# Optimization experiments

Measured on AMD Instinct MI355X. Metric: run time of the kernel, lower is better.

## Reference

```python
import jax, jax.numpy as jnp
import numpy as np

C = 64          # num_channels
NB = 8          # num_bessel
NE = 10         # num_elements
N_NODES = 20000
N_EDGES = 320000

def _silu_norm():
    # e3nn normalize2mom constant for silu: 1/sqrt(E[silu(Z)^2]), Z~N(0,1)
    x, w = np.polynomial.hermite.hermgauss(100)
    z = np.sqrt(2.0) * x
    f = z / (1.0 + np.exp(-z))
    m2 = float(np.sum(w * f * f) / np.sqrt(np.pi))
    return np.float32(1.0 / np.sqrt(m2))

C_SILU = _silu_norm()
SQRT3 = np.float32(np.sqrt(3.0))
SQRT2 = np.float32(np.sqrt(2.0))
INV_SQRT_C = np.float32(1.0 / np.sqrt(C))
INV_SQRT_2C = np.float32(1.0 / np.sqrt(2 * C))
INV_SQRT_3C = np.float32(1.0 / np.sqrt(3 * C))
INV_SQRT_NB = np.float32(1.0 / np.sqrt(NB))
INV_SQRT_64 = np.float32(1.0 / np.sqrt(64.0))


def setup_inputs() -> dict:
    key = jax.random.key(0)
    ks = jax.random.split(key, 22)
    n = lambda k, s: jax.random.normal(k, s, dtype=jnp.float32)
    return {
        "node_feats": n(ks[0], (N_NODES, 4 * C)),
        "edge_feats": jax.random.uniform(ks[1], (N_EDGES, NB), dtype=jnp.float32),
        "edge_attrs": n(ks[2], (N_EDGES, 4)),
        "iedges": jax.random.randint(ks[3], (N_EDGES,), 0, N_NODES),
        "jedges": jax.random.randint(ks[4], (N_EDGES,), 0, N_NODES),
        "atomic_numbers": jax.random.randint(ks[5], (N_NODES,), 0, NE),
        "Wup0": n(ks[6], (C, C)), "Wup1": n(ks[7], (C, C)),
        "Wm1": n(ks[8], (NB, 64)), "Wm2": n(ks[9], (64, 64)),
        "Wm3": n(ks[10], (64, 64)), "Wm4": n(ks[11], (64, 5 * C)),
        "Wl0": n(ks[12], (2 * C, C)), "Wl1": n(ks[13], (3 * C, C)),
        "Ws0c1": n(ks[14], (NE, 1, C)), "Ws0c2": n(ks[15], (NE, 2, C)),
        "Ws0c3": n(ks[16], (NE, 2, C)),
        "Ws1c1": n(ks[17], (NE, 1, C)), "Ws1c2": n(ks[18], (NE, 1, C)),
        "Ws1c3": n(ks[19], (NE, 2, C)),
        "Wp0": n(ks[20], (C, C)), "Wp1": n(ks[21], (C, C)),
    }


def reference(node_feats, edge_feats, edge_attrs, iedges, jedges, atomic_numbers,
              Wup0, Wup1, Wm1, Wm2, Wm3, Wm4, Wl0, Wl1,
              Ws0c1, Ws0c2, Ws0c3, Ws1c1, Ws1c2, Ws1c3, Wp0, Wp1):
    Nn = node_feats.shape[0]
    # split irreps: C scalars (0e) then C vectors (1e), channel-major layout
    s = node_feats[:, :C]                       # (N, C)
    v = node_feats[:, C:].reshape(Nn, C, 3)     # (N, C, 3)

    # linear_up: per-l channel mixing, fan-in normalized (e3nn o3.Linear)
    s = (s @ Wup0) * INV_SQRT_C
    v = jnp.einsum('ncm,ck->nkm', v, Wup1) * INV_SQRT_C

    # conv_tp_weights: e3nn FullyConnectedNet [8,64,64,64,5C] with silu
    h = jax.nn.silu(edge_feats @ (Wm1 * INV_SQRT_NB)) * C_SILU
    h = jax.nn.silu(h @ (Wm2 * INV_SQRT_64)) * C_SILU
    h = jax.nn.silu(h @ (Wm3 * INV_SQRT_64)) * C_SILU
    tpw = h @ (Wm4 * INV_SQRT_64)               # (E, 5C)

    # gather sender node features per edge
    xs = s[iedges]                              # (E, C)
    xv = v[iedges]                              # (E, C, 3)
    eas = edge_attrs[:, 0:1]                    # (E, 1) scalar edge attr
    eav = edge_attrs[:, 1:4]                    # (E, 3) vector edge attr

    # 5 uvu CG paths (component-normalized e3nn TensorProduct):
    wa, wb = tpw[:, 0:C], tpw[:, C:2 * C]
    wc, wd, we = tpw[:, 2 * C:3 * C], tpw[:, 3 * C:4 * C], tpw[:, 4 * C:5 * C]
    m0 = wa * xs * eas                                              # 0e x 0e -> 0e
    m1 = wb * jnp.einsum('ecm,em->ec', xv, eav) / SQRT3             # 1e x 1e -> 0e
    m2 = (wc * xs)[:, :, None] * eav[:, None, :]                    # 0e x 1e -> 1e
    m3 = (wd * eas)[:, :, None] * xv                                # 1e x 0e -> 1e
    m4 = we[:, :, None] * jnp.cross(xv, eav[:, None, :]) / SQRT2    # 1e x 1e -> 1e

    # scatter-sum messages to receiver nodes
    msg_s = jax.ops.segment_sum(jnp.concatenate([m0, m1], axis=1), jedges, num_segments=Nn)        # (N, 2C)
    msg_v = jax.ops.segment_sum(jnp.concatenate([m2, m3, m4], axis=1), jedges, num_segments=Nn)    # (N, 3C, 3)

    # linear: middle irreps (2C x 0e + 3C x 1e) -> C x (0e + 1e)
    s2 = (msg_s @ Wl0) * INV_SQRT_2C            # (N, C)
    v2 = jnp.einsum('ncm,ck->nkm', msg_v, Wl1) * INV_SQRT_3C  # (N, C, 3)

    # symmetric (ACE/MACE) contraction, correlation=3, element-dependent weights
    w01 = Ws0c1[atomic_numbers, 0]              # (N, C)
    w02 = Ws0c2[atomic_numbers]                 # (N, 2, C)
    w03 = Ws0c3[atomic_numbers]                 # (N, 2, C)
    w11 = Ws1c1[atomic_numbers, 0]
    w12 = Ws1c2[atomic_numbers, 0]
    w13 = Ws1c3[atomic_numbers]
    vv = jnp.sum(v2 * v2, axis=-1)              # (N, C) = |v|^2 per channel
    out_s = (w01 * s2 + w02[:, 0] * s2 * s2 + w02[:, 1] * vv / SQRT3
             + w03[:, 0] * s2 * s2 * s2 + w03[:, 1] * s2 * vv / SQRT3)
    coef_v = w11 + w12 * s2 + w13[:, 0] * s2 * s2 + w13[:, 1] * vv / SQRT3
    out_v = coef_v[:, :, None] * v2             # (N, C, 3)

    # linearproduct
    so = (out_s @ Wp0) * INV_SQRT_C
    vo = jnp.einsum('ncm,ck->nkm', out_v, Wp1) * INV_SQRT_C
    return jnp.concatenate([so, vo.reshape(Nn, 3 * C)], axis=1)   # (N, 4C)
```

## Files before the change

kernel.cpp:

```cpp
#include <hip/hip_runtime.h>


typedef unsigned short u16;
typedef unsigned int u32;
typedef __attribute__((ext_vector_type(8))) short bf16x8;
typedef __attribute__((ext_vector_type(4))) float f32x4;

#define CW_UP0 0
#define CW_UP1 4096
#define CW_M1  8192
#define CW_M2  8704
#define CW_M3  12800
#define CW_M4  16896
#define CW_L0  37376
#define CW_L1  45568
#define CW_P0  57856
#define CW_P1  61952
#define CW_S01 66048
#define CW_S02 66688
#define CW_S03 67968
#define CW_S11 69248
#define CW_S12 69888
#define CW_S13 70528
#define CW_TOTAL 71808

#define C_SILU     1.6765224f
#define INV_SQRT3  0.57735027f
#define INV_SQRT2  0.70710678f
#define SC_L1      0.35355339f
#define SC_L234    0.125f

#define HS16 72
#define NFRAG 116
#define FW0 60
#define FW1 76
#define FP0 100
#define FP1 108
#define TP 88

__device__ __forceinline__ float b2f(u16 u) {
  union { u32 i; float f; } x; x.i = ((u32)u) << 16; return x.f;
}
__device__ __forceinline__ u16 f2b(float f) {
  union { float f; u32 i; } x; x.f = f;
  u32 i = x.i;
  u32 r = (i + 0x7fffu + ((i >> 16) & 1u)) >> 16;
  return (u16)r;
}
__device__ __forceinline__ float ldf(const void* p, size_t i, int f32) {
  return f32 ? ((const float*)p)[i] : b2f(((const u16*)p)[i]);
}
__device__ __forceinline__ float silu_n(float x) {
  return C_SILU * x / (1.0f + __expf(-x));
}

__global__ void k_detect(const void* nf, int* flag, int* deg, int nN) {
  __shared__ int cnt;
  if (threadIdx.x == 0) cnt = 0;
  __syncthreads();
  const u16* p = (const u16*)nf;
  int wild = 0;
  for (int i = threadIdx.x; i < 4096; i += 256) {
    float ax = fabsf(b2f(p[i]));
    if (!(ax <= 1e10f) || (ax != 0.f && ax < 1e-10f)) wild++;
  }
  atomicAdd(&cnt, wild);
  for (int i = threadIdx.x; i < nN; i += 256) deg[i] = 0;
  __syncthreads();
  if (threadIdx.x == 0) *flag = (cnt > 100) ? 1 : 0;
}

struct WPtrs { const void* p[16]; };

__global__ __launch_bounds__(256) void k_front(
    WPtrs wp, float* __restrict__ cw, u16* __restrict__ bwH,
    u16* __restrict__ bwL, const int* __restrict__ je, int* __restrict__ deg,
    const void* __restrict__ nf, float* __restrict__ sup,
    float* __restrict__ vup, int nN, int nE, int nb0,
    const int* __restrict__ flagp) {
  __shared__ float row[16][256];
  const int f32 = *flagp;
  int bid = blockIdx.x, tid = threadIdx.x;

  if (bid < 281) {
    const int   sizes[16]  = {4096,4096,512,4096,4096,20480,8192,12288,4096,
                              4096,640,1280,1280,640,640,1280};
    const float scales[16] = {0.125f,0.125f,0.35355339f,0.125f,0.125f,0.125f,
                              0.08838835f,0.07216878f,0.125f,0.125f,
                              1.f,1.f,1.f,1.f,1.f,1.f};
    int gid = bid * 256 + tid;
    if (gid >= CW_TOTAL) return;
    int off = gid, seg = 0;
    while (off >= sizes[seg]) { off -= sizes[seg]; seg++; }
    cw[gid] = ldf(wp.p[seg], off, f32) * scales[seg];
  } else if (bid < 513) {
    int gid = (bid - 281) * 256 + tid;
    int f = gid >> 9, idx = gid & 511;
    int l = idx >> 3, j = idx & 7;
    int q = l >> 4, col16 = l & 15;
    float v = 0.f;
    if (f < 4) {
      int k = q * 8 + j, n = f * 16 + col16;
      if (k < 8) v = ldf(wp.p[2], (size_t)k * 64 + n, f32);
    } else if (f < 20) {
      const void* w = (f < 12) ? wp.p[3] : wp.p[4];
      int t = (f < 12) ? f - 4 : f - 12;
      int n = (t >> 1) * 16 + col16, ks = t & 1;
      int k = ks * 32 + q * 8 + j;
      v = ldf(w, (size_t)k * 64 + n, f32);
    } else if (f < 60) {
      int t = f - 20;
      int n = (t >> 1) * 16 + col16, ks = t & 1;
      int k = ks * 32 + q * 8 + j;
      v = ldf(wp.p[5], (size_t)k * 320 + n, f32);
    } else if (f < 76) {
      int t = f - FW0, ks = t >> 2, n = t & 3;
      int k = ks * 32 + q * 8 + j;
      v = ldf(wp.p[6], (size_t)k * 64 + n * 16 + col16, f32) * 0.08838835f;
    } else if (f < 100) {
      int t = f - FW1, ks = t >> 2, n = t & 3;
      int k = ks * 32 + q * 8 + j;
      v = ldf(wp.p[7], (size_t)k * 64 + n * 16 + col16, f32) * 0.07216878f;
    } else if (f < 108) {
      int t = f - FP0, ks = t >> 2, n = t & 3;
      int k = ks * 32 + q * 8 + j;
      v = ldf(wp.p[8], (size_t)k * 64 + n * 16 + col16, f32) * 0.125f;
    } else {
      int t = f - FP1, ks = t >> 2, n = t & 3;
      int k = ks * 32 + q * 8 + j;
      v = ldf(wp.p[9], (size_t)k * 64 + n * 16 + col16, f32) * 0.125f;
    }
    u16 hi = f2b(v);
    u16 lo = f2b(v - b2f(hi));
    size_t o = (size_t)f * 512 + (size_t)l * 8 + j;
    bwH[o] = hi;
    bwL[o] = lo;
  } else if (bid < nb0) {
    int e = (bid - 513) * 256 + tid;
    if (e < nE) atomicAdd(&deg[je[e]], 1);
  } else {
    int w = tid >> 6, l = tid & 63;
    int nb = (bid - nb0) * 16 + w * 4;
#pragma unroll
    for (int nl = 0; nl < 4; nl++) {
      int n = nb + nl;
      int nn = n < nN ? n : 0;
#pragma unroll
      for (int t = 0; t < 4; t++)
        row[w * 4 + nl][t * 64 + l] = ldf(nf, (size_t)nn * 256 + t * 64 + l, f32);
    }
    float sacc[4] = {0.f, 0.f, 0.f, 0.f};
    float v0[4] = {0.f, 0.f, 0.f, 0.f};
    float v1[4] = {0.f, 0.f, 0.f, 0.f};
    float v2[4] = {0.f, 0.f, 0.f, 0.f};
#pragma unroll 4
    for (int c = 0; c < 64; c++) {
      float w0 = ldf(wp.p[0], (size_t)c * 64 + l, f32);
      float w1 = ldf(wp.p[1], (size_t)c * 64 + l, f32);
#pragma unroll
      for (int nl = 0; nl < 4; nl++) {
        const float* rw = row[w * 4 + nl];
        sacc[nl] += rw[c] * w0;
        v0[nl] += rw[64 + c * 3 + 0] * w1;
        v1[nl] += rw[64 + c * 3 + 1] * w1;
        v2[nl] += rw[64 + c * 3 + 2] * w1;
      }
    }
#pragma unroll
    for (int nl = 0; nl < 4; nl++) {
      int n = nb + nl;
      if (n < nN) {
        sup[(size_t)n * 64 + l] = sacc[nl] * 0.125f;
        vup[((size_t)n * 3 + 0) * 64 + l] = v0[nl] * 0.125f;
        vup[((size_t)n * 3 + 1) * 64 + l] = v1[nl] * 0.125f;
        vup[((size_t)n * 3 + 2) * 64 + l] = v2[nl] * 0.125f;
      }
    }
  }
}

__global__ __launch_bounds__(256) void k_scan(const int* __restrict__ deg,
                                              int* __restrict__ offs,
                                              int* __restrict__ cursor, int nN) {
  __shared__ int wsum[8];
  int t = threadIdx.x;
  int lane = t & 63, wv = t >> 6;
  int base = 0;
  for (int c0 = 0; c0 < nN; c0 += 256) {
    int i = c0 + t;
    int v = (i < nN) ? deg[i] : 0;
    int s = v;
#pragma unroll
    for (int off = 1; off < 64; off <<= 1) {
      int x = __shfl_up(s, off);
      if (lane >= off) s += x;
    }
    if (lane == 63) wsum[wv] = s;
    __syncthreads();
    if (t == 0) {
      int r = 0;
#pragma unroll
      for (int ww = 0; ww < 4; ww++) { int x = wsum[ww]; wsum[ww] = r; r += x; }
      wsum[4] = r;
    }
    __syncthreads();
    int excl = base + wsum[wv] + s - v;
    if (i < nN) { offs[i] = excl; cursor[i] = excl; }
    base += wsum[4];
    __syncthreads();
  }
  if (t == 0) offs[nN] = base;
}

__global__ __launch_bounds__(256) void k_scatter2(
    const int* __restrict__ je, const int* __restrict__ ie,
    const void* __restrict__ ea, const void* __restrict__ ef,
    int* __restrict__ cursor, int* __restrict__ iSlot,
    float4* __restrict__ eaSlot, float4* __restrict__ efSlot, int nE,
    const int* __restrict__ flagp) {
  const int f32 = *flagp;
  int e = blockIdx.x * 256 + threadIdx.x;
  if (e >= nE) return;
  int pos = atomicAdd(&cursor[je[e]], 1);
  iSlot[pos] = ie[e];
  float4 av;
  float4 f0, f1;
  if (f32) {
    av = ((const float4*)ea)[e];
    f0 = ((const float4*)ef)[(size_t)e * 2];
    f1 = ((const float4*)ef)[(size_t)e * 2 + 1];
  } else {
    uint2 r = ((const uint2*)ea)[e];
    av = make_float4(b2f(r.x & 0xffff), b2f(r.x >> 16),
                     b2f(r.y & 0xffff), b2f(r.y >> 16));
    uint4 u = ((const uint4*)ef)[e];
    f0 = make_float4(b2f(u.x & 0xffff), b2f(u.x >> 16),
                     b2f(u.y & 0xffff), b2f(u.y >> 16));
    f1 = make_float4(b2f(u.z & 0xffff), b2f(u.z >> 16),
                     b2f(u.w & 0xffff), b2f(u.w >> 16));
  }
  eaSlot[pos] = av;
  efSlot[(size_t)pos * 2] = f0;
  efSlot[(size_t)pos * 2 + 1] = f1;
}

__global__ __launch_bounds__(192) void k_mlp4(
    const float4* __restrict__ efSlot, const int* __restrict__ offs,
    const u16* __restrict__ bwH, const u16* __restrict__ bwL,
    u16* __restrict__ tpw, int gn0, int gn1, int capEff) {
  __shared__ u16 H[3][64 * HS16];
  int tid = threadIdx.x;
  int w = tid >> 6, l = tid & 63;
  int m = l & 15, q = l >> 4;
  int base = offs[gn0];
  int cnt = offs[gn1] - base;
  int lim = cnt < capEff ? cnt : capEff;
  int tb = (blockIdx.x * 3 + w) * 64;
  if (tb >= lim) return;
  u16* Hw = H[w];

  bf16x8 zero8 = {0,0,0,0,0,0,0,0};
  bf16x8 A1h[4], A1l[4];
#pragma unroll
  for (int t = 0; t < 4; t++) { A1h[t] = zero8; A1l[t] = zero8; }
  if (q == 0) {
#pragma unroll
    for (int t = 0; t < 4; t++) {
      int s = tb + t * 16 + m; if (s > lim - 1) s = lim - 1;
      float4 q0 = efSlot[((size_t)(base + s)) * 2];
      float4 q1 = efSlot[((size_t)(base + s)) * 2 + 1];
      float v[8] = {q0.x, q0.y, q0.z, q0.w, q1.x, q1.y, q1.z, q1.w};
      bf16x8 hi, lo;
#pragma unroll
      for (int j = 0; j < 8; j++) {
        u16 h = f2b(v[j]);
        hi[j] = (short)h;
        lo[j] = (short)f2b(v[j] - b2f(h));
      }
      A1h[t] = hi; A1l[t] = lo;
    }
  }
#pragma unroll
  for (int n = 0; n < 4; n++) {
    bf16x8 Bh = *(const bf16x8*)(bwH + (size_t)n * 512 + (size_t)l * 8);
    bf16x8 Bl = *(const bf16x8*)(bwL + (size_t)n * 512 + (size_t)l * 8);
#pragma unroll
    for (int t = 0; t < 4; t++) {
      f32x4 c = (f32x4){0.f, 0.f, 0.f, 0.f};
      c = __builtin_amdgcn_mfma_f32_16x16x32_bf16(A1h[t], Bh, c, 0, 0, 0);
      c = __builtin_amdgcn_mfma_f32_16x16x32_bf16(A1l[t], Bh, c, 0, 0, 0);
      c = __builtin_amdgcn_mfma_f32_16x16x32_bf16(A1h[t], Bl, c, 0, 0, 0);
#pragma unroll
      for (int r = 0; r < 4; r++)
        Hw[(t * 16 + q * 4 + r) * HS16 + n * 16 + m] =
            f2b(silu_n(c[r] * SC_L1));
    }
  }

#pragma unroll
  for (int layer = 0; layer < 2; layer++) {
    int fragBase = 4 + layer * 8;
    bf16x8 Ah[2][4];
#pragma unroll
    for (int ks = 0; ks < 2; ks++)
#pragma unroll
      for (int t = 0; t < 4; t++)
        Ah[ks][t] = *(const bf16x8*)(Hw + (t * 16 + m) * HS16 + ks * 32 + q * 8);
#pragma unroll
    for (int n = 0; n < 4; n++) {
      bf16x8 B0h = *(const bf16x8*)(bwH + (size_t)(fragBase + n * 2 + 0) * 512 +
                                    (size_t)l * 8);
      bf16x8 B0l = *(const bf16x8*)(bwL + (size_t)(fragBase + n * 2 + 0) * 512 +
                                    (size_t)l * 8);
      bf16x8 B1h = *(const bf16x8*)(bwH + (size_t)(fragBase + n * 2 + 1) * 512 +
                                    (size_t)l * 8);
      bf16x8 B1l = *(const bf16x8*)(bwL + (size_t)(fragBase + n * 2 + 1) * 512 +
                                    (size_t)l * 8);
#pragma unroll
      for (int t = 0; t < 4; t++) {
        f32x4 c = (f32x4){0.f, 0.f, 0.f, 0.f};
        c = __builtin_amdgcn_mfma_f32_16x16x32_bf16(Ah[0][t], B0h, c, 0, 0, 0);
        c = __builtin_amdgcn_mfma_f32_16x16x32_bf16(Ah[0][t], B0l, c, 0, 0, 0);
        c = __builtin_amdgcn_mfma_f32_16x16x32_bf16(Ah[1][t], B1h, c, 0, 0, 0);
        c = __builtin_amdgcn_mfma_f32_16x16x32_bf16(Ah[1][t], B1l, c, 0, 0, 0);
#pragma unroll
        for (int r = 0; r < 4; r++)
          Hw[(t * 16 + q * 4 + r) * HS16 + n * 16 + m] =
              f2b(silu_n(c[r] * SC_L234));
      }
    }
  }

  {
    bf16x8 Ah[2][4];
#pragma unroll
    for (int ks = 0; ks < 2; ks++)
#pragma unroll
      for (int t = 0; t < 4; t++)
        Ah[ks][t] = *(const bf16x8*)(Hw + (t * 16 + m) * HS16 + ks * 32 + q * 8);
    for (int c4 = 0; c4 < 5; c4++) {
#pragma unroll
      for (int nn2 = 0; nn2 < 4; nn2++) {
        int n = c4 * 4 + nn2;
        bf16x8 B0h = *(const bf16x8*)(bwH + (size_t)(20 + n * 2 + 0) * 512 +
                                      (size_t)l * 8);
        bf16x8 B0l = *(const bf16x8*)(bwL + (size_t)(20 + n * 2 + 0) * 512 +
                                      (size_t)l * 8);
        bf16x8 B1h = *(const bf16x8*)(bwH + (size_t)(20 + n * 2 + 1) * 512 +
                                      (size_t)l * 8);
        bf16x8 B1l = *(const bf16x8*)(bwL + (size_t)(20 + n * 2 + 1) * 512 +
                                      (size_t)l * 8);
#pragma unroll
        for (int t = 0; t < 4; t++) {
          f32x4 c = (f32x4){0.f, 0.f, 0.f, 0.f};
          c = __builtin_amdgcn_mfma_f32_16x16x32_bf16(Ah[0][t], B0h, c, 0, 0, 0);
          c = __builtin_amdgcn_mfma_f32_16x16x32_bf16(Ah[0][t], B0l, c, 0, 0, 0);
          c = __builtin_amdgcn_mfma_f32_16x16x32_bf16(Ah[1][t], B1h, c, 0, 0, 0);
          c = __builtin_amdgcn_mfma_f32_16x16x32_bf16(Ah[1][t], B1l, c, 0, 0, 0);
#pragma unroll
          for (int r = 0; r < 4; r++)
            Hw[(t * 16 + q * 4 + r) * HS16 + nn2 * 16 + m] =
                f2b(c[r] * SC_L234);
        }
      }
      int r8 = l >> 3, cc = l & 7;
#pragma unroll
      for (int i = 0; i < 8; i++) {
        int row = i * 8 + r8;
        int srow = tb + row;
        if (srow < lim) {
          uint4 v = *(const uint4*)(Hw + row * HS16 + cc * 8);
          *(uint4*)(tpw + (size_t)srow * 320 + c4 * 64 + cc * 8) = v;
        }
      }
    }
  }
}

__global__ __launch_bounds__(256) void k_gather6(
    const int* __restrict__ iSlot, const float4* __restrict__ eaSlot,
    const int* __restrict__ offs, const float* __restrict__ sup,
    const float* __restrict__ vup, const u16* __restrict__ tpw,
    u16* __restrict__ msgSh, u16* __restrict__ msgSl,
    u16* __restrict__ msgVh, u16* __restrict__ msgVl,
    int gn0, int gn1, int capEff) {
  int w = threadIdx.x >> 6, l = threadIdx.x & 63;
  int n = gn0 + blockIdx.x * 4 + w;
  if (n >= gn1) return;
  int gbase = offs[gn0];
  int start = offs[n];
  int deg = offs[n + 1] - start;
  int avail = capEff - (start - gbase);
  int dmax = deg < avail ? deg : avail;
  if (dmax < 0) dmax = 0;

  float as0 = 0.f, as1 = 0.f;
  float av[9];
#pragma unroll
  for (int m = 0; m < 9; m++) av[m] = 0.f;

  for (int c0 = 0; c0 < dmax; c0 += 64) {
    int rem = dmax - c0;
    int cend = rem < 64 ? rem : 64;
    int iA = 0;
    float4 eaA = make_float4(0.f, 0.f, 0.f, 0.f);
    if (l < cend) {
      iA = iSlot[start + c0 + l];
      eaA = eaSlot[start + c0 + l];
    }
    for (int qq = 0; qq < cend; qq++) {
      int i = __shfl(iA, qq);
      float eas = __shfl(eaA.x, qq);
      float ev0 = __shfl(eaA.y, qq);
      float ev1 = __shfl(eaA.z, qq);
      float ev2 = __shfl(eaA.w, qq);
      const u16* tp = tpw + (size_t)(start - gbase + c0 + qq) * 320;
      float wa  = b2f(tp[l]);
      float wbv = b2f(tp[64 + l]);
      float wc  = b2f(tp[128 + l]);
      float wd  = b2f(tp[192 + l]);
      float we_ = b2f(tp[256 + l]);
      float xs  = sup[(size_t)i * 64 + l];
      float xv0 = vup[((size_t)i * 3 + 0) * 64 + l];
      float xv1 = vup[((size_t)i * 3 + 1) * 64 + l];
      float xv2 = vup[((size_t)i * 3 + 2) * 64 + l];
      float dot = xv0 * ev0 + xv1 * ev1 + xv2 * ev2;
      as0 += wa * xs * eas;
      as1 += wbv * dot * INV_SQRT3;
      float wcxs = wc * xs;
      float wde  = wd * eas;
      float wef  = we_ * INV_SQRT2;
      av[0] += wcxs * ev0; av[1] += wcxs * ev1; av[2] += wcxs * ev2;
      av[3] += wde * xv0;  av[4] += wde * xv1;  av[5] += wde * xv2;
      av[6] += wef * (xv1 * ev2 - xv2 * ev1);
      av[7] += wef * (xv2 * ev0 - xv0 * ev2);
      av[8] += wef * (xv0 * ev1 - xv1 * ev0);
    }
  }

  {
    u16 h0 = f2b(as0), h1 = f2b(as1);
    msgSh[(size_t)n * 128 + l] = h0;
    msgSh[(size_t)n * 128 + 64 + l] = h1;
    msgSl[(size_t)n * 128 + l] = f2b(as0 - b2f(h0));
    msgSl[(size_t)n * 128 + 64 + l] = f2b(as1 - b2f(h1));
  }
#pragma unroll
  for (int c = 0; c < 3; c++) {
#pragma unroll
    for (int b = 0; b < 3; b++) {
      float x = av[b * 3 + c];
      u16 h = f2b(x);
      size_t o = (size_t)n * 576 + c * 192 + b * 64 + l;
      msgVh[o] = h;
      msgVl[o] = f2b(x - b2f(h));
    }
  }
}

__global__ __launch_bounds__(256) void k_post2(
    const u16* __restrict__ msgSh, const u16* __restrict__ msgSl,
    const u16* __restrict__ msgVh, const u16* __restrict__ msgVl,
    const int* __restrict__ an, const float* __restrict__ cw,
    const u16* __restrict__ bwH, const u16* __restrict__ bwL,
    void* __restrict__ out, int nN, const int* __restrict__ flagp) {
  __shared__ u16 Thi[16][TP];
  __shared__ u16 Tlo[16][TP];
  const int f32 = *flagp;
  int tid = threadIdx.x;
  int w = tid >> 6, l = tid & 63;
  int m = l & 15, q = l >> 4;
  int n0 = blockIdx.x * 16;
  int rowA = n0 + m; if (rowA > nN - 1) rowA = nN - 1;

  f32x4 s2 = (f32x4){0.f, 0.f, 0.f, 0.f};
#pragma unroll
  for (int ks = 0; ks < 4; ks++) {
    bf16x8 Bh = *(const bf16x8*)(bwH + (size_t)(FW0 + ks * 4 + w) * 512 +
                                 (size_t)l * 8);
    bf16x8 Bl = *(const bf16x8*)(bwL + (size_t)(FW0 + ks * 4 + w) * 512 +
                                 (size_t)l * 8);
    bf16x8 Ah = *(const bf16x8*)(msgSh + (size_t)rowA * 128 + ks * 32 + q * 8);
    bf16x8 Al = *(const bf16x8*)(msgSl + (size_t)rowA * 128 + ks * 32 + q * 8);
    s2 = __builtin_amdgcn_mfma_f32_16x16x32_bf16(Ah, Bh, s2, 0, 0, 0);
    s2 = __builtin_amdgcn_mfma_f32_16x16x32_bf16(Al, Bh, s2, 0, 0, 0);
    s2 = __builtin_amdgcn_mfma_f32_16x16x32_bf16(Ah, Bl, s2, 0, 0, 0);
  }

  f32x4 v2[3];
#pragma unroll
  for (int c = 0; c < 3; c++) v2[c] = (f32x4){0.f, 0.f, 0.f, 0.f};
#pragma unroll
  for (int ks = 0; ks < 6; ks++) {
    bf16x8 Bh = *(const bf16x8*)(bwH + (size_t)(FW1 + ks * 4 + w) * 512 +
                                 (size_t)l * 8);
    bf16x8 Bl = *(const bf16x8*)(bwL + (size_t)(FW1 + ks * 4 + w) * 512 +
                                 (size_t)l * 8);
#pragma unroll
    for (int c = 0; c < 3; c++) {
      size_t o = (size_t)rowA * 576 + c * 192 + ks * 32 + q * 8;
      bf16x8 Ah = *(const bf16x8*)(msgVh + o);
      bf16x8 Al = *(const bf16x8*)(msgVl + o);
      v2[c] = __builtin_amdgcn_mfma_f32_16x16x32_bf16(Ah, Bh, v2[c], 0, 0, 0);
      v2[c] = __builtin_amdgcn_mfma_f32_16x16x32_bf16(Al, Bh, v2[c], 0, 0, 0);
      v2[c] = __builtin_amdgcn_mfma_f32_16x16x32_bf16(Ah, Bl, v2[c], 0, 0, 0);
    }
  }

  float os[4], ov0[4], ov1[4], ov2[4];
#pragma unroll
  for (int r = 0; r < 4; r++) {
    int node = n0 + q * 4 + r;
    int nc = node > nN - 1 ? nN - 1 : node;
    int a = an[nc];
    int ch = w * 16 + m;
    float s2v = s2[r];
    float va = v2[0][r], vb = v2[1][r], vc = v2[2][r];
    float vv = va * va + vb * vb + vc * vc;
    float w01  = cw[CW_S01 + a * 64 + ch];
    float w02a = cw[CW_S02 + a * 128 + ch];
    float w02b = cw[CW_S02 + a * 128 + 64 + ch];
    float w03a = cw[CW_S03 + a * 128 + ch];
    float w03b = cw[CW_S03 + a * 128 + 64 + ch];
    float w11  = cw[CW_S11 + a * 64 + ch];
    float w12  = cw[CW_S12 + a * 64 + ch];
    float w13a = cw[CW_S13 + a * 128 + ch];
    float w13b = cw[CW_S13 + a * 128 + 64 + ch];
    float s2sq = s2v * s2v;
    float vvs = vv * INV_SQRT3;
    os[r] = w01 * s2v + w02a * s2sq + w02b * vvs + w03a * s2sq * s2v +
            w03b * s2v * vvs;
    float coef = w11 + w12 * s2v + w13a * s2sq + w13b * vvs;
    ov0[r] = coef * va;
    ov1[r] = coef * vb;
    ov2[r] = coef * vc;
  }

#define POST2_G2(SRC, FB, STORE_S, COMP)                                       \
  {                                                                            \
    __syncthreads();                                                           \
    _Pragma("unroll")                                                          \
    for (int r = 0; r < 4; r++) {                                              \
      float x = SRC[r];                                                        \
      u16 h = f2b(x);                                                          \
      Thi[q * 4 + r][w * 16 + m] = h;                                          \
      Tlo[q * 4 + r][w * 16 + m] = f2b(x - b2f(h));                            \
    }                                                                          \
    __syncthreads();                                                           \
    f32x4 d = (f32x4){0.f, 0.f, 0.f, 0.f};                                     \
    _Pragma("unroll")                                                          \
    for (int ks = 0; ks < 2; ks++) {                                           \
      bf16x8 Bh = *(const bf16x8*)(bwH + (size_t)(FB + ks * 4 + w) * 512 +     \
                                   (size_t)l * 8);                             \
      bf16x8 Bl = *(const bf16x8*)(bwL + (size_t)(FB + ks * 4 + w) * 512 +     \
                                   (size_t)l * 8);                             \
      bf16x8 Ah = *(const bf16x8*)(&Thi[m][ks * 32 + q * 8]);                  \
      bf16x8 Al = *(const bf16x8*)(&Tlo[m][ks * 32 + q * 8]);                  \
      d = __builtin_amdgcn_mfma_f32_16x16x32_bf16(Ah, Bh, d, 0, 0, 0);         \
      d = __builtin_amdgcn_mfma_f32_16x16x32_bf16(Al, Bh, d, 0, 0, 0);         \
      d = __builtin_amdgcn_mfma_f32_16x16x32_bf16(Ah, Bl, d, 0, 0, 0);         \
    }                                                                          \
    _Pragma("unroll")                                                          \
    for (int r = 0; r < 4; r++) {                                              \
      int node = n0 + q * 4 + r;                                               \
      if (node < nN) {                                                         \
        int ch = w * 16 + m;                                                   \
        size_t basep = (size_t)node * 256;                                     \
        size_t oidx = STORE_S ? (basep + ch) : (basep + 64 + ch * 3 + COMP);   \
        if (f32) ((float*)out)[oidx] = d[r];                                   \
        else ((u16*)out)[oidx] = f2b(d[r]);                                    \
      }                                                                        \
    }                                                                          \
  }

  POST2_G2(os, FP0, 1, 0)
  POST2_G2(ov0, FP1, 0, 0)
  POST2_G2(ov1, FP1, 0, 1)
  POST2_G2(ov2, FP1, 0, 2)
#undef POST2_G2
}

extern "C" void kernel_launch(void* const* d_in, const int* in_sizes, int n_in,
                              void* d_out, int out_size, void* d_ws,
                              size_t ws_size, hipStream_t stream) {
  const void* nf = d_in[0];
  const void* ef = d_in[1];
  const void* ea = d_in[2];
  const int* ie = (const int*)d_in[3];
  const int* je = (const int*)d_in[4];
  const int* an = (const int*)d_in[5];
  int nN = in_sizes[0] / 256;
  int nE = in_sizes[3];

  size_t intCnt = (size_t)3 * nN + 1 + nE;
  intCnt = (intCnt + 3) & ~(size_t)3;
  int* deg    = (int*)d_ws;
  int* offs   = deg + nN;
  int* cursor = offs + nN + 1;
  int* iSlot  = cursor + nN;
  float* cw   = (float*)d_ws + intCnt;
  float* sup  = cw + CW_TOTAL;
  float* vup  = sup + (size_t)nN * 64;
  int* flag   = (int*)(vup + (size_t)nN * 192);

  size_t msgByte = (size_t)((char*)(flag + 1) - (char*)d_ws);
  msgByte = (msgByte + 15) & ~(size_t)15;
  u16* msgSh = (u16*)((char*)d_ws + msgByte);
  u16* msgSl = msgSh + (size_t)nN * 128;
  u16* msgVh = msgSl + (size_t)nN * 128;
  u16* msgVl = msgVh + (size_t)nN * 576;

  size_t eaByte = msgByte + (size_t)nN * 1408 * 2;
  eaByte = (eaByte + 15) & ~(size_t)15;
  float4* eaSlot = (float4*)((char*)d_ws + eaByte);
  float4* efSlot = eaSlot + nE;
  size_t bwByte = eaByte + (size_t)nE * 16 + (size_t)nE * 32;
  u16* bwH = (u16*)((char*)d_ws + bwByte);
  u16* bwL = bwH + (size_t)NFRAG * 512;
  size_t tpwByte = bwByte + (size_t)NFRAG * 512 * 2 * 2;
  tpwByte = (tpwByte + 15) & ~(size_t)15;
  u16* tpw = (u16*)((char*)d_ws + tpwByte);
  size_t capE = (ws_size > tpwByte) ? (ws_size - tpwByte) / 640 : 0;

  int G = 64;
  int nodesPer = (nN + 63) / 64;
  for (int g = 1; g <= 64; g++) {
    int npg = (nN + g - 1) / g;
    size_t worst = (size_t)npg * nE / nN + 6000;
    if (worst <= capE) { G = g; nodesPer = npg; break; }
  }
  int capEff = (int)((size_t)nodesPer * nE / nN + 6000);
  if ((size_t)capEff > capE) capEff = (int)capE;

  k_detect<<<1, 256, 0, stream>>>(nf, flag, deg, nN);

  WPtrs wp;
  const int widx[16] = {6, 7, 8, 9, 10, 11, 12, 13, 20, 21,
                        14, 15, 16, 17, 18, 19};
  for (int i = 0; i < 16; i++) wp.p[i] = d_in[widx[i]];

  int histNB = (nE + 255) / 256;
  int nb0 = 513 + histNB;
  int nupNB = (nN + 15) / 16;
  k_front<<<nb0 + nupNB, 256, 0, stream>>>(wp, cw, bwH, bwL, je, deg, nf,
                                           sup, vup, nN, nE, nb0, flag);
  k_scan<<<1, 256, 0, stream>>>(deg, offs, cursor, nN);
  k_scatter2<<<(nE + 255) / 256, 256, 0, stream>>>(je, ie, ea, ef, cursor,
                                                   iSlot, eaSlot, efSlot, nE,
                                                   flag);

  for (int g = 0; g < G; g++) {
    int gn0 = g * nodesPer;
    if (gn0 >= nN) break;
    int gn1 = gn0 + nodesPer; if (gn1 > nN) gn1 = nN;
    int mlpBlocks = (capEff + 191) / 192;
    k_mlp4<<<mlpBlocks, 192, 0, stream>>>(efSlot, offs, bwH, bwL, tpw,
                                          gn0, gn1, capEff);
    int gBlocks = (gn1 - gn0 + 3) / 4;
    k_gather6<<<gBlocks, 256, 0, stream>>>(iSlot, eaSlot, offs, sup, vup,
                                           tpw, msgSh, msgSl, msgVh, msgVl,
                                           gn0, gn1, capEff);
  }
  int postNB = (nN + 15) / 16;
  k_post2<<<postNB, 256, 0, stream>>>(msgSh, msgSl, msgVh, msgVl, an, cw,
                                      bwH, bwL, d_out, nN, flag);
}
```

Baseline: 512.7 us.

## Fuse edge MLP with message gather using segmented atomic accumulation

Result: slower. 597.3 us (+16.5%).

```diff
diff --git a/kernel.cpp b/kernel.cpp
--- a/kernel.cpp
+++ b/kernel.cpp
@@ -52,6 +52,17 @@
 }
 __device__ __forceinline__ float silu_n(float x) {
   return C_SILU * x / (1.0f + __expf(-x));
+}
+__device__ __forceinline__ void mk8(const float* ap, bf16x8& Ah, bf16x8& Al) {
+  float4 f0 = *(const float4*)ap;
+  float4 f1 = *(const float4*)(ap + 4);
+  float v[8] = {f0.x, f0.y, f0.z, f0.w, f1.x, f1.y, f1.z, f1.w};
+#pragma unroll
+  for (int j = 0; j < 8; j++) {
+    u16 h = f2b(v[j]);
+    Ah[j] = (short)h;
+    Al[j] = (short)f2b(v[j] - b2f(h));
+  }
 }
 
 __global__ void k_detect(const void* nf, int* flag, int* deg, int nN) {
@@ -215,14 +226,22 @@
 __global__ __launch_bounds__(256) void k_scatter2(
     const int* __restrict__ je, const int* __restrict__ ie,
     const void* __restrict__ ea, const void* __restrict__ ef,
-    int* __restrict__ cursor, int* __restrict__ iSlot,
-    float4* __restrict__ eaSlot, float4* __restrict__ efSlot, int nE,
+    int* __restrict__ cursor, int* __restrict__ iSlot, int* __restrict__ jSlot,
+    float4* __restrict__ eaSlot, float4* __restrict__ efSlot,
+    float* __restrict__ msgAll, int nE, int nN,
     const int* __restrict__ flagp) {
   const int f32 = *flagp;
+  size_t tot = (size_t)nN * 704;
+  size_t stride = (size_t)gridDim.x * 256;
+  for (size_t k2 = (size_t)blockIdx.x * 256 + threadIdx.x; k2 < tot; k2 += stride)
+    msgAll[k2] = 0.f;
+
   int e = blockIdx.x * 256 + threadIdx.x;
   if (e >= nE) return;
-  int pos = atomicAdd(&cursor[je[e]], 1);
+  int jn = je[e];
+  int pos = atomicAdd(&cursor[jn], 1);
   iSlot[pos] = ie[e];
+  jSlot[pos] = jn;
   float4 av;
   float4 f0, f1;
   if (f32) {
@@ -244,20 +263,28 @@
   efSlot[(size_t)pos * 2 + 1] = f1;
 }
 
-__global__ __launch_bounds__(192) void k_mlp4(
-    const float4* __restrict__ efSlot, const int* __restrict__ offs,
+__global__ __launch_bounds__(192) void k_mlp5(
+    const float4* __restrict__ efSlot, const int* __restrict__ iSlot,
+    const int* __restrict__ jSlot, const float4* __restrict__ eaSlot,
+    const float* __restrict__ sup, const float* __restrict__ vup,
     const u16* __restrict__ bwH, const u16* __restrict__ bwL,
-    u16* __restrict__ tpw, int gn0, int gn1, int capEff) {
+    float* __restrict__ msgS, float* __restrict__ msgV, int nE) {
   __shared__ u16 H[3][64 * HS16];
   int tid = threadIdx.x;
   int w = tid >> 6, l = tid & 63;
   int m = l & 15, q = l >> 4;
-  int base = offs[gn0];
-  int cnt = offs[gn1] - base;
-  int lim = cnt < capEff ? cnt : capEff;
   int tb = (blockIdx.x * 3 + w) * 64;
-  if (tb >= lim) return;
+  if (tb >= nE) return;
+  int cend = nE - tb; if (cend > 64) cend = 64;
   u16* Hw = H[w];
+
+  int iA = 0, jA = 0;
+  float4 eaA = make_float4(0.f, 0.f, 0.f, 0.f);
+  if (l < cend) {
+    iA = iSlot[tb + l];
+    jA = jSlot[tb + l];
+    eaA = eaSlot[tb + l];
+  }
 
   bf16x8 zero8 = {0,0,0,0,0,0,0,0};
   bf16x8 A1h[4], A1l[4];
@@ -266,9 +293,9 @@
   if (q == 0) {
 #pragma unroll
     for (int t = 0; t < 4; t++) {
-      int s = tb + t * 16 + m; if (s > lim - 1) s = lim - 1;
-      float4 q0 = efSlot[((size_t)(base + s)) * 2];
-      float4 q1 = efSlot[((size_t)(base + s)) * 2 + 1];
+      int s = tb + t * 16 + m; if (s > nE - 1) s = nE - 1;
+      float4 q0 = efSlot[(size_t)s * 2];
+      float4 q1 = efSlot[(size_t)s * 2 + 1];
       float v[8] = {q0.x, q0.y, q0.z, q0.w, q1.x, q1.y, q1.z, q1.w};
       bf16x8 hi, lo;
 #pragma unroll
@@ -338,6 +365,7 @@
 #pragma unroll
       for (int t = 0; t < 4; t++)
         Ah[ks][t] = *(const bf16x8*)(Hw + (t * 16 + m) * HS16 + ks * 32 + q * 8);
+#pragma unroll
     for (int c4 = 0; c4 < 5; c4++) {
 #pragma unroll
       for (int nn2 = 0; nn2 < 4; nn2++) {
@@ -363,104 +391,71 @@
                 f2b(c[r] * SC_L234);
         }
       }
-      int r8 = l >> 3, cc = l & 7;
-#pragma unroll
-      for (int i = 0; i < 8; i++) {
-        int row = i * 8 + r8;
-        int srow = tb + row;
-        if (srow < lim) {
-          uint4 v = *(const uint4*)(Hw + row * HS16 + cc * 8);
-          *(uint4*)(tpw + (size_t)srow * 320 + c4 * 64 + cc * 8) = v;
+      float a0 = 0.f, a1 = 0.f, a2 = 0.f;
+      int cur = __shfl(jA, 0);
+      for (int s = 0; s < cend; s++) {
+        int nd = __shfl(jA, s);
+        if (nd != cur) {
+          if (c4 == 0) atomicAdd(&msgS[(size_t)cur * 128 + l], a0);
+          else if (c4 == 1) atomicAdd(&msgS[(size_t)cur * 128 + 64 + l], a0);
+          else {
+            int b = c4 - 2;
+            atomicAdd(&msgV[(size_t)cur * 576 + 0 * 192 + b * 64 + l], a0);
+            atomicAdd(&msgV[(size_t)cur * 576 + 1 * 192 + b * 64 + l], a1);
+            atomicAdd(&msgV[(size_t)cur * 576 + 2 * 192 + b * 64 + l], a2);
+          }
+          a0 = a1 = a2 = 0.f;
+          cur = nd;
+        }
+        int i = __shfl(iA, s);
+        float wv = b2f(Hw[s * HS16 + l]);
+        if (c4 == 0) {
+          float eas = __shfl(eaA.x, s);
+          a0 += wv * sup[(size_t)i * 64 + l] * eas;
+        } else if (c4 == 1) {
+          float e0 = __shfl(eaA.y, s), e1 = __shfl(eaA.z, s),
+                e2 = __shfl(eaA.w, s);
+          float dot = vup[((size_t)i * 3 + 0) * 64 + l] * e0 +
+                      vup[((size_t)i * 3 + 1) * 64 + l] * e1 +
+                      vup[((size_t)i * 3 + 2) * 64 + l] * e2;
+          a0 += wv * dot * INV_SQRT3;
+        } else if (c4 == 2) {
+          float e0 = __shfl(eaA.y, s), e1 = __shfl(eaA.z, s),
+                e2 = __shfl(eaA.w, s);
+          float t = wv * sup[(size_t)i * 64 + l];
+          a0 += t * e0; a1 += t * e1; a2 += t * e2;
+        } else if (c4 == 3) {
+          float eas = __shfl(eaA.x, s);
+          float t = wv * eas;
+          a0 += t * vup[((size_t)i * 3 + 0) * 64 + l];
+          a1 += t * vup[((size_t)i * 3 + 1) * 64 + l];
+          a2 += t * vup[((size_t)i * 3 + 2) * 64 + l];
+        } else {
+          float e0 = __shfl(eaA.y, s), e1 = __shfl(eaA.z, s),
+                e2 = __shfl(eaA.w, s);
+          float xv0 = vup[((size_t)i * 3 + 0) * 64 + l];
+          float xv1 = vup[((size_t)i * 3 + 1) * 64 + l];
+          float xv2 = vup[((size_t)i * 3 + 2) * 64 + l];
+          float t = wv * INV_SQRT2;
+          a0 += t * (xv1 * e2 - xv2 * e1);
+          a1 += t * (xv2 * e0 - xv0 * e2);
+          a2 += t * (xv0 * e1 - xv1 * e0);
         }
       }
-    }
-  }
-}
-
-__global__ __launch_bounds__(256) void k_gather6(
-    const int* __restrict__ iSlot, const float4* __restrict__ eaSlot,
-    const int* __restrict__ offs, const float* __restrict__ sup,
-    const float* __restrict__ vup, const u16* __restrict__ tpw,
-    u16* __restrict__ msgSh, u16* __restrict__ msgSl,
-    u16* __restrict__ msgVh, u16* __restrict__ msgVl,
-    int gn0, int gn1, int capEff) {
-  int w = threadIdx.x >> 6, l = threadIdx.x & 63;
-  int n = gn0 + blockIdx.x * 4 + w;
-  if (n >= gn1) return;
-  int gbase = offs[gn0];
-  int start = offs[n];
-  int deg = offs[n + 1] - start;
-  int avail = capEff - (start - gbase);
-  int dmax = deg < avail ? deg : avail;
-  if (dmax < 0) dmax = 0;
-
-  float as0 = 0.f, as1 = 0.f;
-  float av[9];
-#pragma unroll
-  for (int m = 0; m < 9; m++) av[m] = 0.f;
-
-  for (int c0 = 0; c0 < dmax; c0 += 64) {
-    int rem = dmax - c0;
-    int cend = rem < 64 ? rem : 64;
-    int iA = 0;
-    float4 eaA = make_float4(0.f, 0.f, 0.f, 0.f);
-    if (l < cend) {
-      iA = iSlot[start + c0 + l];
-      eaA = eaSlot[start + c0 + l];
-    }
-    for (int qq = 0; qq < cend; qq++) {
-      int i = __shfl(iA, qq);
-      float eas = __shfl(eaA.x, qq);
-      float ev0 = __shfl(eaA.y, qq);
-      float ev1 = __shfl(eaA.z, qq);
-      float ev2 = __shfl(eaA.w, qq);
-      const u16* tp = tpw + (size_t)(start - gbase + c0 + qq) * 320;
-      float wa  = b2f(tp[l]);
-      float wbv = b2f(tp[64 + l]);
-      float wc  = b2f(tp[128 + l]);
-      float wd  = b2f(tp[192 + l]);
-      float we_ = b2f(tp[256 + l]);
-      float xs  = sup[(size_t)i * 64 + l];
-      float xv0 = vup[((size_t)i * 3 + 0) * 64 + l];
-      float xv1 = vup[((size_t)i * 3 + 1) * 64 + l];
-      float xv2 = vup[((size_t)i * 3 + 2) * 64 + l];
-      float dot = xv0 * ev0 + xv1 * ev1 + xv2 * ev2;
-      as0 += wa * xs * eas;
-      as1 += wbv * dot * INV_SQRT3;
-      float wcxs = wc * xs;
-      float wde  = wd * eas;
-      float wef  = we_ * INV_SQRT2;
-      av[0] += wcxs * ev0; av[1] += wcxs * ev1; av[2] += wcxs * ev2;
-      av[3] += wde * xv0;  av[4] += wde * xv1;  av[5] += wde * xv2;
-      av[6] += wef * (xv1 * ev2 - xv2 * ev1);
-      av[7] += wef * (xv2 * ev0 - xv0 * ev2);
-      av[8] += wef * (xv0 * ev1 - xv1 * ev0);
-    }
-  }
-
-  {
-    u16 h0 = f2b(as0), h1 = f2b(as1);
-    msgSh[(size_t)n * 128 + l] = h0;
-    msgSh[(size_t)n * 128 + 64 + l] = h1;
-    msgSl[(size_t)n * 128 + l] = f2b(as0 - b2f(h0));
-    msgSl[(size_t)n * 128 + 64 + l] = f2b(as1 - b2f(h1));
-  }
-#pragma unroll
-  for (int c = 0; c < 3; c++) {
-#pragma unroll
-    for (int b = 0; b < 3; b++) {
-      float x = av[b * 3 + c];
-      u16 h = f2b(x);
-      size_t o = (size_t)n * 576 + c * 192 + b * 64 + l;
-      msgVh[o] = h;
-      msgVl[o] = f2b(x - b2f(h));
+      if (c4 == 0) atomicAdd(&msgS[(size_t)cur * 128 + l], a0);
+      else if (c4 == 1) atomicAdd(&msgS[(size_t)cur * 128 + 64 + l], a0);
+      else {
+        int b = c4 - 2;
+        atomicAdd(&msgV[(size_t)cur * 576 + 0 * 192 + b * 64 + l], a0);
+        atomicAdd(&msgV[(size_t)cur * 576 + 1 * 192 + b * 64 + l], a1);
+        atomicAdd(&msgV[(size_t)cur * 576 + 2 * 192 + b * 64 + l], a2);
+      }
     }
   }
 }
 
 __global__ __launch_bounds__(256) void k_post2(
-    const u16* __restrict__ msgSh, const u16* __restrict__ msgSl,
-    const u16* __restrict__ msgVh, const u16* __restrict__ msgVl,
+    const float* __restrict__ msgS, const float* __restrict__ msgV,
     const int* __restrict__ an, const float* __restrict__ cw,
     const u16* __restrict__ bwH, const u16* __restrict__ bwL,
     void* __restrict__ out, int nN, const int* __restrict__ flagp) {
@@ -480,8 +475,8 @@
                                  (size_t)l * 8);
     bf16x8 Bl = *(const bf16x8*)(bwL + (size_t)(FW0 + ks * 4 + w) * 512 +
                                  (size_t)l * 8);
-    bf16x8 Ah = *(const bf16x8*)(msgSh + (size_t)rowA * 128 + ks * 32 + q * 8);
-    bf16x8 Al = *(const bf16x8*)(msgSl + (size_t)rowA * 128 + ks * 32 + q * 8);
+    bf16x8 Ah, Al;
+    mk8(msgS + (size_t)rowA * 128 + ks * 32 + q * 8, Ah, Al);
     s2 = __builtin_amdgcn_mfma_f32_16x16x32_bf16(Ah, Bh, s2, 0, 0, 0);
     s2 = __builtin_amdgcn_mfma_f32_16x16x32_bf16(Al, Bh, s2, 0, 0, 0);
     s2 = __builtin_amdgcn_mfma_f32_16x16x32_bf16(Ah, Bl, s2, 0, 0, 0);
@@ -498,9 +493,8 @@
                                  (size_t)l * 8);
 #pragma unroll
     for (int c = 0; c < 3; c++) {
-      size_t o = (size_t)rowA * 576 + c * 192 + ks * 32 + q * 8;
-      bf16x8 Ah = *(const bf16x8*)(msgVh + o);
-      bf16x8 Al = *(const bf16x8*)(msgVl + o);
+      bf16x8 Ah, Al;
+      mk8(msgV + (size_t)rowA * 576 + c * 192 + ks * 32 + q * 8, Ah, Al);
       v2[c] = __builtin_amdgcn_mfma_f32_16x16x32_bf16(Ah, Bh, v2[c], 0, 0, 0);
       v2[c] = __builtin_amdgcn_mfma_f32_16x16x32_bf16(Al, Bh, v2[c], 0, 0, 0);
       v2[c] = __builtin_amdgcn_mfma_f32_16x16x32_bf16(Ah, Bl, v2[c], 0, 0, 0);
@@ -592,12 +586,13 @@
   int nN = in_sizes[0] / 256;
   int nE = in_sizes[3];
 
-  size_t intCnt = (size_t)3 * nN + 1 + nE;
+  size_t intCnt = (size_t)3 * nN + 1 + 2 * (size_t)nE;
   intCnt = (intCnt + 3) & ~(size_t)3;
   int* deg    = (int*)d_ws;
   int* offs   = deg + nN;
   int* cursor = offs + nN + 1;
   int* iSlot  = cursor + nN;
+  int* jSlot  = iSlot + nE;
   float* cw   = (float*)d_ws + intCnt;
   float* sup  = cw + CW_TOTAL;
   float* vup  = sup + (size_t)nN * 64;
@@ -605,32 +600,16 @@
 
   size_t msgByte = (size_t)((char*)(flag + 1) - (char*)d_ws);
   msgByte = (msgByte + 15) & ~(size_t)15;
-  u16* msgSh = (u16*)((char*)d_ws + msgByte);
-  u16* msgSl = msgSh + (size_t)nN * 128;
-  u16* msgVh = msgSl + (size_t)nN * 128;
-  u16* msgVl = msgVh + (size_t)nN * 576;
-
-  size_t eaByte = msgByte + (size_t)nN * 1408 * 2;
+  float* msgS = (float*)((char*)d_ws + msgByte);
+  float* msgV = msgS + (size_t)nN * 128;
+
+  size_t eaByte = msgByte + (size_t)nN * 704 * 4;
   eaByte = (eaByte + 15) & ~(size_t)15;
   float4* eaSlot = (float4*)((char*)d_ws + eaByte);
   float4* efSlot = eaSlot + nE;
   size_t bwByte = eaByte + (size_t)nE * 16 + (size_t)nE * 32;
   u16* bwH = (u16*)((char*)d_ws + bwByte);
   u16* bwL = bwH + (size_t)NFRAG * 512;
-  size_t tpwByte = bwByte + (size_t)NFRAG * 512 * 2 * 2;
-  tpwByte = (tpwByte + 15) & ~(size_t)15;
-  u16* tpw = (u16*)((char*)d_ws + tpwByte);
-  size_t capE = (ws_size > tpwByte) ? (ws_size - tpwByte) / 640 : 0;
-
-  int G = 64;
-  int nodesPer = (nN + 63) / 64;
-  for (int g = 1; g <= 64; g++) {
-    int npg = (nN + g - 1) / g;
-    size_t worst = (size_t)npg * nE / nN + 6000;
-    if (worst <= capE) { G = g; nodesPer = npg; break; }
-  }
-  int capEff = (int)((size_t)nodesPer * nE / nN + 6000);
-  if ((size_t)capEff > capE) capEff = (int)capE;
 
   k_detect<<<1, 256, 0, stream>>>(nf, flag, deg, nN);
 
@@ -646,22 +625,13 @@
                                            sup, vup, nN, nE, nb0, flag);
   k_scan<<<1, 256, 0, stream>>>(deg, offs, cursor, nN);
   k_scatter2<<<(nE + 255) / 256, 256, 0, stream>>>(je, ie, ea, ef, cursor,
-                                                   iSlot, eaSlot, efSlot, nE,
-                                                   flag);
-
-  for (int g = 0; g < G; g++) {
-    int gn0 = g * nodesPer;
-    if (gn0 >= nN) break;
-    int gn1 = gn0 + nodesPer; if (gn1 > nN) gn1 = nN;
-    int mlpBlocks = (capEff + 191) / 192;
-    k_mlp4<<<mlpBlocks, 192, 0, stream>>>(efSlot, offs, bwH, bwL, tpw,
-                                          gn0, gn1, capEff);
-    int gBlocks = (gn1 - gn0 + 3) / 4;
-    k_gather6<<<gBlocks, 256, 0, stream>>>(iSlot, eaSlot, offs, sup, vup,
-                                           tpw, msgSh, msgSl, msgVh, msgVl,
-                                           gn0, gn1, capEff);
-  }
+                                                   iSlot, jSlot, eaSlot,
+                                                   efSlot, msgS, nE, nN, flag);
+
+  int mlpBlocks = (nE + 191) / 192;
+  k_mlp5<<<mlpBlocks, 192, 0, stream>>>(efSlot, iSlot, jSlot, eaSlot, sup,
+                                        vup, bwH, bwL, msgS, msgV, nE);
   int postNB = (nN + 15) / 16;
-  k_post2<<<postNB, 256, 0, stream>>>(msgSh, msgSl, msgVh, msgVl, an, cw,
-                                      bwH, bwL, d_out, nN, flag);
-}
+  k_post2<<<postNB, 256, 0, stream>>>(msgS, msgV, an, cw, bwH, bwL, d_out,
+                                      nN, flag);
+}
```
